# Optimization experiments

Hardware: AMD Instinct MI355X
Metric: run time of the kernel (lower is better)

Reference implementation:

```python
import jax, jax.numpy as jnp
import numpy as np


def setup_inputs() -> dict:
    key = jax.random.key(0)
    k1, k2 = jax.random.split(key)
    B, C, H, W = 8, 256, 64, 64
    G, KS = 8, 5
    x = jax.random.normal(k1, (B, C, H, W), dtype=jnp.float32)
    w = jax.random.normal(k2, (B, G, KS * KS, H, W), dtype=jnp.float32)
    return {"x": x, "w": w}


def reference(x, w):
    # x: [B, C, H, W]; w: [B, G, ks*ks, H, W] per-pixel dynamic depthwise weights
    B, C, H, W = x.shape
    G = w.shape[1]
    K2 = w.shape[2]
    ks = int(round(K2 ** 0.5))
    pad = (ks - 1) // 2
    Cg = C // G
    xp = jnp.pad(x, ((0, 0), (0, 0), (pad, pad), (pad, pad)))
    # Extract ks*ks shifted views: [B, C, ks*ks, H, W]
    patches = jnp.stack(
        [xp[:, :, i:i + H, j:j + W] for i in range(ks) for j in range(ks)],
        axis=2,
    )
    patches = patches.reshape(B, G, Cg, K2, H, W)
    # weighted patch sum per pixel, weights shared within each channel group
    out = jnp.einsum('bgckhw,bgkhw->bgchw', patches, w)
    return out.reshape(B, C, H, W)
```

## Files before the change

kernel.cpp:

```cpp
#include <hip/hip_runtime.h>


#define B_ 8
#define C_ 256
#define G_ 8
#define CG_ 32
#define H_ 64
#define W_ 64
#define K2_ 25
#define HW_ (H_ * W_)
#define NCH 8
#define PITCH 66
#define BUFW 544
#define WAVEW (2 * BUFW)

__global__ __launch_bounds__(256, 2) void ska_kernel(
    const float* __restrict__ x, const float* __restrict__ w,
    float* __restrict__ out) {
  __shared__ float lds[4 * WAVEW];
  const int tid = threadIdx.x;
  const int lane = tid & 63;
  const int wv = tid >> 6;
  const int j = lane & 15;
  const int r = lane >> 4;
  const int blk = blockIdx.x;
  const int chunk = blk & 3;
  const int band = (blk >> 2) & 3;
  const int g = (blk >> 4) & 7;
  const int b = blk >> 7;
  const int h0w = band * 16 + wv * 4;
  const int h = h0w + r;
  const int wcol = j * 4;
  const int wbase = wv * WAVEW;

  if (lane < 18) {
    int idx;
    if (lane < 2) idx = lane;
    else idx = 2 + ((lane - 2) >> 1) * PITCH + 64 + ((lane - 2) & 1);
    lds[wbase + idx] = 0.0f;
    lds[wbase + BUFW + idx] = 0.0f;
  }

  float wk[K2_][4];
  const float* wb =
      w + (size_t)(b * G_ + g) * K2_ * HW_ + (size_t)h * W_ + wcol;
#pragma unroll
  for (int k = 0; k < K2_; ++k) {
    const int di = k / 5 - 2;
    const int dj = k % 5 - 2;
    const int hh = h + di;
    const bool rowok = (unsigned)hh < (unsigned)H_;
    const float4 wq = *(const float4*)(wb + (size_t)k * HW_);
#pragma unroll
    for (int t = 0; t < 4; ++t) {
      const int cc = wcol + t + dj;
      const bool ok = rowok && ((unsigned)cc < (unsigned)W_);
      wk[k][t] = ok ? ((const float*)&wq)[t] : 0.0f;
    }
  }

  const int scol = (lane & 15) * 4;
  const int sr = lane >> 4;
  const int srow0 = min(max(h0w - 2 + sr, 0), H_ - 1);
  const int srow1 = min(max(h0w + 2 + sr, 0), H_ - 1);
  const int woff0 = wbase + 2 + sr * PITCH + scol;
  const int woff1 = wbase + 2 + (4 + sr) * PITCH + scol;

  const size_t chan0 = (size_t)(b * C_ + g * CG_ + chunk * NCH) * HW_;
  const float* xc = x + chan0;
  float* ob = out + chan0 + (size_t)h * W_ + wcol;

  float4 q0 = *(const float4*)(xc + srow0 * W_ + scol);
  float4 q1 = *(const float4*)(xc + srow1 * W_ + scol);

  for (int c = 0; c < NCH; ++c) {
    const int cn = min(c + 1, NCH - 1);
    const float* xn = xc + (size_t)cn * HW_;
    const float4 p0 = *(const float4*)(xn + srow0 * W_ + scol);
    const float4 p1 = *(const float4*)(xn + srow1 * W_ + scol);

    __builtin_amdgcn_wave_barrier();
    const int bo = (c & 1) * BUFW;
    *(float2*)&lds[woff0 + bo] = make_float2(q0.x, q0.y);
    *(float2*)&lds[woff0 + bo + 2] = make_float2(q0.z, q0.w);
    *(float2*)&lds[woff1 + bo] = make_float2(q1.x, q1.y);
    *(float2*)&lds[woff1 + bo + 2] = make_float2(q1.z, q1.w);
    __builtin_amdgcn_wave_barrier();

    alignas(16) float acc[4] = {0.f, 0.f, 0.f, 0.f};
#pragma unroll
    for (int di = 0; di < 5; ++di) {
      const int base = wbase + bo + (r + di) * PITCH + wcol;
      alignas(16) float xr[8];
      *(float2*)&xr[0] = *(const float2*)&lds[base];
      *(float2*)&xr[2] = *(const float2*)&lds[base + 2];
      *(float2*)&xr[4] = *(const float2*)&lds[base + 4];
      *(float2*)&xr[6] = *(const float2*)&lds[base + 6];
#pragma unroll
      for (int dj = 0; dj < 5; ++dj) {
        const int k = di * 5 + dj;
#pragma unroll
        for (int t = 0; t < 4; ++t) {
          acc[t] = fmaf(xr[t + dj], wk[k][t], acc[t]);
        }
      }
    }
    *(float4*)(ob + (size_t)c * HW_) = *(const float4*)acc;
    q0 = p0;
    q1 = p1;
  }
}

extern "C" void kernel_launch(void* const* d_in, const int* in_sizes, int n_in,
                              void* d_out, int out_size, void* d_ws,
                              size_t ws_size, hipStream_t stream) {
  const float* x = (const float*)d_in[0];
  const float* w = (const float*)d_in[1];
  float* out = (float*)d_out;
  ska_kernel<<<dim3(1024), dim3(256), 0, stream>>>(x, w, out);
}
```

Baseline: 115.3 us.

## Stage all channel tiles in LDS and stream weights per kernel row

Each block now loads all 8 channels of its 16-row band (with halo) into shared memory with a single block-wide barrier, instead of each wave double-buffering one channel at a time. The loops are swapped so the outer loop is the kernel row and the inner loop is the channel. Only 5 weight vectors are held at a time, and the next row's weights are prefetched, which replaces the 100-register weight array and is meant to allow 3 blocks per SM. The cost is 8 accumulator vectors per thread, a full-block sync, and no overlap between the global loads and compute inside a block. Halo zeros are now written explicitly and the column bounds come from the zero-padded LDS columns.

Result: slower. 125.6 us (+9.0%).

```diff
diff --git a/kernel.cpp b/kernel.cpp
--- a/kernel.cpp
+++ b/kernel.cpp
@@ -10,105 +10,114 @@
 #define K2_ 25
 #define HW_ (H_ * W_)
 #define NCH 8
-#define PITCH 66
-#define BUFW 544
-#define WAVEW (2 * BUFW)
+#define NROWS 20
+#define PITCH 68
+#define CHSTRIDE 1364
 
-__global__ __launch_bounds__(256, 2) void ska_kernel(
+__global__ __launch_bounds__(256, 3) void ska_kernel(
     const float* __restrict__ x, const float* __restrict__ w,
     float* __restrict__ out) {
-  __shared__ float lds[4 * WAVEW];
+  __shared__ __align__(16) float lds[NCH * CHSTRIDE];
   const int tid = threadIdx.x;
-  const int lane = tid & 63;
-  const int wv = tid >> 6;
-  const int j = lane & 15;
-  const int r = lane >> 4;
+  const int lr = tid >> 4;
+  const int j = tid & 15;
+  const int wcol = j * 4;
+
   const int blk = blockIdx.x;
-  const int chunk = blk & 3;
-  const int band = (blk >> 2) & 3;
-  const int g = (blk >> 4) & 7;
-  const int b = blk >> 7;
-  const int h0w = band * 16 + wv * 4;
-  const int h = h0w + r;
-  const int wcol = j * 4;
-  const int wbase = wv * WAVEW;
+  const int band = blk & 3;
+  const int g = (blk >> 2) & 7;
+  const int b = (blk >> 5) & 7;
+  const int chunk = blk >> 8;
 
-  if (lane < 18) {
-    int idx;
-    if (lane < 2) idx = lane;
-    else idx = 2 + ((lane - 2) >> 1) * PITCH + 64 + ((lane - 2) & 1);
-    lds[wbase + idx] = 0.0f;
-    lds[wbase + BUFW + idx] = 0.0f;
-  }
+  const int h0 = band * 16;
+  const int h = h0 + lr;
 
-  float wk[K2_][4];
   const float* wb =
       w + (size_t)(b * G_ + g) * K2_ * HW_ + (size_t)h * W_ + wcol;
+  float4 wcur0 = *(const float4*)(wb + (size_t)0 * HW_);
+  float4 wcur1 = *(const float4*)(wb + (size_t)1 * HW_);
+  float4 wcur2 = *(const float4*)(wb + (size_t)2 * HW_);
+  float4 wcur3 = *(const float4*)(wb + (size_t)3 * HW_);
+  float4 wcur4 = *(const float4*)(wb + (size_t)4 * HW_);
+
 #pragma unroll
-  for (int k = 0; k < K2_; ++k) {
-    const int di = k / 5 - 2;
-    const int dj = k % 5 - 2;
-    const int hh = h + di;
-    const bool rowok = (unsigned)hh < (unsigned)H_;
-    const float4 wq = *(const float4*)(wb + (size_t)k * HW_);
-#pragma unroll
-    for (int t = 0; t < 4; ++t) {
-      const int cc = wcol + t + dj;
-      const bool ok = rowok && ((unsigned)cc < (unsigned)W_);
-      wk[k][t] = ok ? ((const float*)&wq)[t] : 0.0f;
+  for (int it = 0; it < 3; ++it) {
+    const int i = tid + it * 256;
+    if (i < NCH * 82) {
+      const int c = i / 82;
+      const int p = i - c * 82;
+      const int word =
+          (p < 2) ? p : (66 + ((p - 2) >> 2) * PITCH + ((p - 2) & 3));
+      lds[c * CHSTRIDE + word] = 0.0f;
     }
   }
 
-  const int scol = (lane & 15) * 4;
-  const int sr = lane >> 4;
-  const int srow0 = min(max(h0w - 2 + sr, 0), H_ - 1);
-  const int srow1 = min(max(h0w + 2 + sr, 0), H_ - 1);
-  const int woff0 = wbase + 2 + sr * PITCH + scol;
-  const int woff1 = wbase + 2 + (4 + sr) * PITCH + scol;
-
   const size_t chan0 = (size_t)(b * C_ + g * CG_ + chunk * NCH) * HW_;
   const float* xc = x + chan0;
-  float* ob = out + chan0 + (size_t)h * W_ + wcol;
+#pragma unroll
+  for (int c = 0; c < NCH; ++c) {
+#pragma unroll
+    for (int it = 0; it < 2; ++it) {
+      const int i = tid + it * 256;
+      if (i < NROWS * 16) {
+        const int rl = i >> 4;
+        const int q = i & 15;
+        const int gr = h0 - 2 + rl;
+        float4 v = make_float4(0.f, 0.f, 0.f, 0.f);
+        if ((unsigned)gr < (unsigned)H_)
+          v = *(const float4*)(xc + (size_t)c * HW_ + gr * W_ + q * 4);
+        const int wo = c * CHSTRIDE + 2 + rl * PITCH + q * 4;
+        *(float2*)&lds[wo] = make_float2(v.x, v.y);
+        *(float2*)&lds[wo + 2] = make_float2(v.z, v.w);
+      }
+    }
+  }
 
-  float4 q0 = *(const float4*)(xc + srow0 * W_ + scol);
-  float4 q1 = *(const float4*)(xc + srow1 * W_ + scol);
+  __syncthreads();
 
+  alignas(16) float acc[NCH][4];
+#pragma unroll
   for (int c = 0; c < NCH; ++c) {
-    const int cn = min(c + 1, NCH - 1);
-    const float* xn = xc + (size_t)cn * HW_;
-    const float4 p0 = *(const float4*)(xn + srow0 * W_ + scol);
-    const float4 p1 = *(const float4*)(xn + srow1 * W_ + scol);
+    acc[c][0] = 0.f; acc[c][1] = 0.f; acc[c][2] = 0.f; acc[c][3] = 0.f;
+  }
 
-    __builtin_amdgcn_wave_barrier();
-    const int bo = (c & 1) * BUFW;
-    *(float2*)&lds[woff0 + bo] = make_float2(q0.x, q0.y);
-    *(float2*)&lds[woff0 + bo + 2] = make_float2(q0.z, q0.w);
-    *(float2*)&lds[woff1 + bo] = make_float2(q1.x, q1.y);
-    *(float2*)&lds[woff1 + bo + 2] = make_float2(q1.z, q1.w);
-    __builtin_amdgcn_wave_barrier();
-
-    alignas(16) float acc[4] = {0.f, 0.f, 0.f, 0.f};
+  float4 wn0, wn1, wn2, wn3, wn4;
 #pragma unroll
-    for (int di = 0; di < 5; ++di) {
-      const int base = wbase + bo + (r + di) * PITCH + wcol;
+  for (int di = 0; di < 5; ++di) {
+    if (di < 4) {
+      const size_t kb = (size_t)((di + 1) * 5) * HW_;
+      wn0 = *(const float4*)(wb + kb + 0 * HW_);
+      wn1 = *(const float4*)(wb + kb + 1 * HW_);
+      wn2 = *(const float4*)(wb + kb + 2 * HW_);
+      wn3 = *(const float4*)(wb + kb + 3 * HW_);
+      wn4 = *(const float4*)(wb + kb + 4 * HW_);
+    }
+    const int rbase = (lr + di) * PITCH + wcol;
+#pragma unroll
+    for (int c = 0; c < NCH; ++c) {
       alignas(16) float xr[8];
-      *(float2*)&xr[0] = *(const float2*)&lds[base];
-      *(float2*)&xr[2] = *(const float2*)&lds[base + 2];
-      *(float2*)&xr[4] = *(const float2*)&lds[base + 4];
-      *(float2*)&xr[6] = *(const float2*)&lds[base + 6];
+      *(float4*)&xr[0] = *(const float4*)&lds[c * CHSTRIDE + rbase];
+      *(float4*)&xr[4] = *(const float4*)&lds[c * CHSTRIDE + rbase + 4];
 #pragma unroll
       for (int dj = 0; dj < 5; ++dj) {
-        const int k = di * 5 + dj;
-#pragma unroll
-        for (int t = 0; t < 4; ++t) {
-          acc[t] = fmaf(xr[t + dj], wk[k][t], acc[t]);
-        }
+        const float4 wv = (dj == 0) ? wcur0
+                        : (dj == 1) ? wcur1
+                        : (dj == 2) ? wcur2
+                        : (dj == 3) ? wcur3
+                                    : wcur4;
+        acc[c][0] = fmaf(xr[dj + 0], wv.x, acc[c][0]);
+        acc[c][1] = fmaf(xr[dj + 1], wv.y, acc[c][1]);
+        acc[c][2] = fmaf(xr[dj + 2], wv.z, acc[c][2]);
+        acc[c][3] = fmaf(xr[dj + 3], wv.w, acc[c][3]);
       }
     }
-    *(float4*)(ob + (size_t)c * HW_) = *(const float4*)acc;
-    q0 = p0;
-    q1 = p1;
+    wcur0 = wn0; wcur1 = wn1; wcur2 = wn2; wcur3 = wn3; wcur4 = wn4;
   }
+
+  float* ob = out + chan0 + (size_t)h * W_ + wcol;
+#pragma unroll
+  for (int c = 0; c < NCH; ++c)
+    *(float4*)(ob + (size_t)c * HW_) = *(const float4*)acc[c];
 }
 
 extern "C" void kernel_launch(void* const* d_in, const int* in_sizes, int n_in,
```
